# Optimization experiments

Hardware: AMD Instinct MI355X
Metric: run time of the kernel (lower is better)

The kernel has to match this reference:

```python
import jax, jax.numpy as jnp
import numpy as np

B, S, E, H, W = 1, 4096, 1024, 16, 256
D = E // H
SCALE = D ** -0.5


def setup_inputs() -> dict:
    key = jax.random.key(0)
    k1, k2, k3 = jax.random.split(key, 3)
    x = jax.random.normal(k1, (B, S, E), dtype=jnp.float32)
    # torch Linear weight is [out,in]; we store transposed [in,out] so y = x @ w
    w_qkv = jax.random.normal(k2, (E, 3 * E), dtype=jnp.float32) * (E ** -0.5)
    w_out = jax.random.normal(k3, (E, E), dtype=jnp.float32) * (E ** -0.5)
    # sliding-window causal mask: key j allowed for query i iff i-W < j <= i
    q_idx = jnp.arange(S)[:, None]
    k_idx = jnp.arange(S)[None, :]
    allowed_mask = (k_idx <= q_idx) & (k_idx > q_idx - W)  # [S,S] bool
    allowed_mask = allowed_mask[None, None]  # [1,1,S,S]
    return {"x": x, "allowed_mask": allowed_mask, "w_qkv": w_qkv, "w_out": w_out}


def reference(x, allowed_mask, w_qkv, w_out):
    b, s, e = x.shape
    qkv = (x @ w_qkv).reshape(b, s, 3, H, D)
    q, k, v = jnp.moveaxis(qkv, 2, 0)  # each [b,s,H,D]
    q = q.transpose(0, 2, 1, 3)  # [b,H,s,D]
    k = k.transpose(0, 2, 1, 3)
    v = v.transpose(0, 2, 1, 3)
    scores = jnp.einsum('bhsd,bhtd->bhst', q, k) * SCALE  # [b,H,s,s]
    scores = jnp.where(allowed_mask, scores, -jnp.inf)
    attn = jax.nn.softmax(scores, axis=-1)
    out = jnp.einsum('bhst,bhtd->bhsd', attn, v)  # [b,H,s,D]
    out = out.transpose(0, 2, 1, 3).reshape(b, s, e)
    return out @ w_out
```

## Files before the change

kernel.cpp:

```cpp
#include <hip/hip_runtime.h>
#include <hip/hip_bf16.h>

#define S_LEN 4096
#define EMB   1024
#define NH    16
#define HD    64
#define WIN   256
#define SCALE 0.125f

typedef __attribute__((ext_vector_type(8))) short short8;
typedef __attribute__((ext_vector_type(4))) float f32x4;
typedef __attribute__((ext_vector_type(4))) unsigned short us4;

__device__ inline unsigned short f2b(float x) {
    __hip_bfloat16 b = __float2bfloat16(x);
    return *reinterpret_cast<unsigned short*>(&b);
}

__device__ inline void gld_lds16(const unsigned short* g, unsigned short* l) {
    __builtin_amdgcn_global_load_lds(
        (const __attribute__((address_space(1))) unsigned int*)g,
        (__attribute__((address_space(3))) unsigned int*)l,
        16, 0, 0);
}

__device__ inline void transpose_tile(const float* __restrict__ in,
                                      unsigned short* __restrict__ out,
                                      int R, int C, int bx, int by,
                                      unsigned short* t) {
    const int tid = threadIdx.x;
    const int r0 = by * 64, c0 = bx * 64;

    const int rr = tid >> 4, cc = (tid & 15) * 4;
    #pragma unroll
    for (int i = 0; i < 4; ++i) {
        float4 v = *reinterpret_cast<const float4*>(&in[(size_t)(r0 + rr + i * 16) * C + c0 + cc]);
        t[(cc + 0) * 72 + rr + i * 16] = f2b(v.x);
        t[(cc + 1) * 72 + rr + i * 16] = f2b(v.y);
        t[(cc + 2) * 72 + rr + i * 16] = f2b(v.z);
        t[(cc + 3) * 72 + rr + i * 16] = f2b(v.w);
    }
    __syncthreads();

    const int wr = tid >> 2, wk = (tid & 3) * 16;
    #pragma unroll
    for (int p = 0; p < 2; ++p)
        *reinterpret_cast<uint4*>(&out[(size_t)(c0 + wr) * R + r0 + wk + p * 8]) =
            *reinterpret_cast<const uint4*>(&t[wr * 72 + wk + p * 8]);
}

__global__ __launch_bounds__(256) void prep(const float* __restrict__ x,
                                            unsigned short* __restrict__ xb,
                                            const float* __restrict__ w_qkv,
                                            unsigned short* __restrict__ wqkvT,
                                            const float* __restrict__ w_out,
                                            unsigned short* __restrict__ woutT) {
    __shared__ alignas(16) unsigned short t[64 * 72];
    const int b = blockIdx.x;
    if (b < 768) {
        transpose_tile(w_qkv, wqkvT, EMB, 3 * EMB, b % 48, b / 48, t);
    } else if (b < 1024) {
        const int bb = b - 768;
        transpose_tile(w_out, woutT, EMB, EMB, bb & 15, bb >> 4, t);
    } else {
        const size_t tt = (size_t)(b - 1024) * 256 + threadIdx.x;
        const float4* s4 = reinterpret_cast<const float4*>(x) + tt * 4;
        float4 v0 = s4[0], v1 = s4[1], v2 = s4[2], v3 = s4[3];
        us4 p0 = {f2b(v0.x), f2b(v0.y), f2b(v0.z), f2b(v0.w)};
        us4 p1 = {f2b(v1.x), f2b(v1.y), f2b(v1.z), f2b(v1.w)};
        us4 p2 = {f2b(v2.x), f2b(v2.y), f2b(v2.z), f2b(v2.w)};
        us4 p3 = {f2b(v3.x), f2b(v3.y), f2b(v3.z), f2b(v3.w)};
        us4* d = reinterpret_cast<us4*>(xb) + tt * 4;
        d[0] = p0; d[1] = p1; d[2] = p2; d[3] = p3;
    }
}

template <int MODE, int BN>
__global__ __launch_bounds__(256) void gemm_bt(const unsigned short* __restrict__ A,
                                               const unsigned short* __restrict__ Bt,
                                               void* __restrict__ Cout,
                                               unsigned short* __restrict__ vT,
                                               int M, int N, int K) {
    constexpr int SMEM_ELEMS = (MODE == 1) ? 17408 : 8192 + BN * 64;
    constexpr int NJ = BN / 32;
    __shared__ alignas(16) unsigned short smem[SMEM_ELEMS];
    unsigned short* As = smem;
    unsigned short* Bs = smem + 8192;

    const int tid  = threadIdx.x;
    const int lane = tid & 63;
    const int w    = tid >> 6;
    const int quad = lane >> 4;
    const int l16  = lane & 15;

    const int m0 = blockIdx.y * 128;
    const int n0 = blockIdx.x * BN;
    const int m_off = (w & 1) * 64;
    const int n_off = (w >> 1) * (BN / 2);

    const int s_row = tid >> 3;
    const int s_c0  = tid & 7;

    f32x4 acc[4][NJ];
    #pragma unroll
    for (int i = 0; i < 4; ++i)
        #pragma unroll
        for (int j = 0; j < NJ; ++j)
            acc[i][j] = (f32x4){0.f, 0.f, 0.f, 0.f};

    for (int bk = 0; bk < K; bk += 64) {
        __syncthreads();
        #pragma unroll
        for (int p = 0; p < 4; ++p) {
            const int row = p * 32 + s_row;
            const int c   = s_c0 ^ (row & 7);
            gld_lds16(A + (size_t)(m0 + row) * K + bk + c * 8,
                      As + (p * 256 + w * 64) * 8);
        }
        #pragma unroll
        for (int p = 0; p < BN / 32; ++p) {
            const int row = p * 32 + s_row;
            const int c   = s_c0 ^ (row & 7);
            gld_lds16(Bt + (size_t)(n0 + row) * K + bk + c * 8,
                      Bs + (p * 256 + w * 64) * 8);
        }
        __syncthreads();

        #pragma unroll
        for (int ks = 0; ks < 2; ++ks) {
            short8 af[4], bf[NJ];
            #pragma unroll
            for (int i = 0; i < 4; ++i) {
                const int r = m_off + i * 16 + l16;
                af[i] = *reinterpret_cast<const short8*>(
                    &As[r * 64 + ((ks * 4 + quad) ^ (r & 7)) * 8]);
            }
            #pragma unroll
            for (int j = 0; j < NJ; ++j) {
                const int r = n_off + j * 16 + l16;
                bf[j] = *reinterpret_cast<const short8*>(
                    &Bs[r * 64 + ((ks * 4 + quad) ^ (r & 7)) * 8]);
            }
            #pragma unroll
            for (int i = 0; i < 4; ++i)
                #pragma unroll
                for (int j = 0; j < NJ; ++j)
                    acc[i][j] = __builtin_amdgcn_mfma_f32_16x16x32_bf16(
                        af[i], bf[j], acc[i][j], 0, 0, 0);
        }
    }

    if (MODE == 0) {
        float* C = (float*)Cout;
        #pragma unroll
        for (int i = 0; i < 4; ++i)
            #pragma unroll
            for (int r = 0; r < 4; ++r) {
                const size_t row = m0 + m_off + i * 16 + quad * 4 + r;
                #pragma unroll
                for (int j = 0; j < NJ; ++j)
                    C[row * N + n0 + n_off + j * 16 + l16] = acc[i][j][r];
            }
    } else if (n0 < 2048) {
        const float sc = (n0 < 1024) ? SCALE : 1.0f;
        unsigned short* C = (unsigned short*)Cout;
        #pragma unroll
        for (int i = 0; i < 4; ++i)
            #pragma unroll
            for (int r = 0; r < 4; ++r) {
                const size_t row = m0 + m_off + i * 16 + quad * 4 + r;
                #pragma unroll
                for (int j = 0; j < NJ; ++j)
                    C[row * N + n0 + n_off + j * 16 + l16] = f2b(acc[i][j][r] * sc);
            }
    } else {
        __syncthreads();
        #pragma unroll
        for (int i = 0; i < 4; ++i) {
            const int ss = m_off + i * 16 + quad * 4;
            #pragma unroll
            for (int j = 0; j < NJ; ++j) {
                const int dd = n_off + j * 16 + l16;
                us4 pk = {f2b(acc[i][j][0]), f2b(acc[i][j][1]),
                          f2b(acc[i][j][2]), f2b(acc[i][j][3])};
                *reinterpret_cast<us4*>(&smem[dd * 136 + ss]) = pk;
            }
        }
        __syncthreads();
        #pragma unroll
        for (int p = 0; p < 8; ++p) {
            const int t  = p * 256 + tid;
            const int dd = t >> 4;
            const int sc2 = (t & 15) * 8;
            *reinterpret_cast<uint4*>(&vT[(size_t)(n0 - 2048 + dd) * S_LEN + m0 + sc2]) =
                *reinterpret_cast<const uint4*>(&smem[dd * 136 + sc2]);
        }
    }
}

__global__ __launch_bounds__(512) void gemm_qkv(const unsigned short* __restrict__ A,
                                                const unsigned short* __restrict__ Bt,
                                                unsigned short* __restrict__ C,
                                                unsigned short* __restrict__ vT) {
    __shared__ alignas(16) unsigned short smem[65536];

    constexpr int K = EMB;
    const int tid  = threadIdx.x;
    const int lane = tid & 63;
    const int w    = tid >> 6;
    const int quad = lane >> 4;
    const int l16  = lane & 15;
    const int wr   = w >> 2, wc = w & 3;
    const int wm0  = wr * 128, wn0 = wc * 64;

    const int raw = blockIdx.x;
    const int s   = (raw & 7) * 24 + (raw >> 3);
    const int by  = s / 12, bx = s % 12;
    const int m0  = by * 256, n0 = bx * 256;

    const int srow = tid >> 2;
    const int scp  = tid & 3;
    const int sc4  = scp ^ ((srow >> 1) & 3);
    const unsigned short* pA = A  + (size_t)(m0 + srow) * K + sc4 * 8;
    const unsigned short* pB = Bt + (size_t)(n0 + srow) * K + sc4 * 8;
    const int dls = (w * 64) * 8;

    auto STAGE = [&](int q) {
        unsigned short* dA = smem + ((q >> 1) & 1) * 32768 + (q & 1) * 8192 + dls;
        unsigned short* dB = dA + 16384;
        const int gk = q * 32;
        gld_lds16(pA + gk, dA);
        gld_lds16(pA + (size_t)128 * K + gk, dA + 4096);
        gld_lds16(pB + gk, dB);
        gld_lds16(pB + (size_t)128 * K + gk, dB + 4096);
    };

    auto BASE = [&](int p) -> const unsigned short* {
        return smem + ((p >> 1) & 1) * 32768 + (p & 1) * 8192;
    };

    const int cpf = quad ^ ((l16 >> 1) & 3);
    const int oA  = (wm0 + l16) * 32 + cpf * 8;
    const int oB  = (wn0 + l16) * 32 + cpf * 8;

    f32x4 acc[8][4];
    #pragma unroll
    for (int i = 0; i < 8; ++i)
        #pragma unroll
        for (int j = 0; j < 4; ++j)
            acc[i][j] = (f32x4){0.f, 0.f, 0.f, 0.f};

    short8 afA[8], afB[8];

#define PHASE_RR(p, CUR, NXT, DO_PF, DO_ST) do {                               \
    const unsigned short* Bb_ = BASE(p) + 16384;                               \
    short8 bf[4];                                                              \
    _Pragma("unroll")                                                          \
    for (int j = 0; j < 4; ++j)                                                \
        bf[j] = *reinterpret_cast<const short8*>(&Bb_[oB + j * 512]);          \
    if (DO_PF) {                                                               \
        const unsigned short* An_ = BASE((p) + 1);                             \
        _Pragma("unroll")                                                      \
        for (int i = 0; i < 8; ++i)                                            \
            NXT[i] = *reinterpret_cast<const short8*>(&An_[oA + i * 512]);     \
    }                                                                          \
    if (DO_ST) STAGE((p) + 3);                                                 \
    __builtin_amdgcn_s_setprio(1);                                             \
    _Pragma("unroll")                                                          \
    for (int j = 0; j < 4; ++j)                                                \
        _Pragma("unroll")                                                      \
        for (int i = 0; i < 8; ++i)                                            \
            acc[i][j] = __builtin_amdgcn_mfma_f32_16x16x32_bf16(               \
                CUR[i], bf[j], acc[i][j], 0, 0, 0);                            \
    __builtin_amdgcn_s_setprio(0);                                             \
} while (0)

    STAGE(0); STAGE(1); STAGE(2);
    asm volatile("s_waitcnt vmcnt(4)" ::: "memory");
    __builtin_amdgcn_s_barrier();
    {
        const unsigned short* A0_ = BASE(0);
        #pragma unroll
        for (int i = 0; i < 8; ++i)
            afA[i] = *reinterpret_cast<const short8*>(&A0_[oA + i * 512]);
    }

    for (int pp = 0; pp < 28; pp += 2) {
        PHASE_RR(pp, afA, afB, true, true);
        asm volatile("s_waitcnt vmcnt(4)" ::: "memory");
        __builtin_amdgcn_s_barrier();
        PHASE_RR(pp + 1, afB, afA, true, true);
        asm volatile("s_waitcnt vmcnt(4)" ::: "memory");
        __builtin_amdgcn_s_barrier();
    }
    PHASE_RR(28, afA, afB, true, true);
    asm volatile("s_waitcnt vmcnt(4)" ::: "memory");
    __builtin_amdgcn_s_barrier();
    PHASE_RR(29, afB, afA, true, false);
    asm volatile("s_waitcnt vmcnt(0)" ::: "memory");
    __builtin_amdgcn_s_barrier();
    PHASE_RR(30, afA, afB, true, false);
    __builtin_amdgcn_s_barrier();
    PHASE_RR(31, afB, afA, false, false);
    __builtin_amdgcn_s_barrier();

#undef PHASE_RR

    const int sec = n0 >> 10;
    if (sec < 2) {
        const float sc = (sec == 0) ? SCALE : 1.0f;
        #pragma unroll
        for (int i = 0; i < 8; ++i) {
            #pragma unroll
            for (int r = 0; r < 4; ++r) {
                const size_t row = (size_t)(m0 + wm0 + i * 16 + quad * 4 + r) * 3072;
                #pragma unroll
                for (int j = 0; j < 4; ++j)
                    C[row + n0 + wn0 + j * 16 + l16] = f2b(acc[i][j][r] * sc);
            }
        }
    } else {
        #pragma unroll
        for (int i = 0; i < 8; ++i) {
            const int ss = wm0 + i * 16 + quad * 4;
            const int sc0 = ss >> 3, se = ss & 7;
            #pragma unroll
            for (int j = 0; j < 4; ++j) {
                const int d = wn0 + j * 16 + l16;
                us4 pk = {f2b(acc[i][j][0]), f2b(acc[i][j][1]),
                          f2b(acc[i][j][2]), f2b(acc[i][j][3])};
                *reinterpret_cast<us4*>(&smem[d * 256 + ((sc0 ^ (d & 31)) << 3) + se]) = pk;
            }
        }
        __builtin_amdgcn_s_barrier();
        const int vb = n0 - 2048;
        #pragma unroll
        for (int rep = 0; rep < 16; ++rep) {
            const int idx = rep * 512 + tid;
            const int d = idx >> 5, scr = idx & 31;
            *reinterpret_cast<uint4*>(&vT[(size_t)(vb + d) * S_LEN + m0 + scr * 8]) =
                *reinterpret_cast<const uint4*>(&smem[d * 256 + ((scr ^ (d & 31)) << 3)]);
        }
    }
}

typedef __attribute__((ext_vector_type(2))) unsigned int u32x2;

template <int PAR>
__device__ __forceinline__ void pv_phase(const u32x2 (&PA)[17], unsigned short* scrw,
                                         const unsigned short* Vt, f32x4 (&acco)[4],
                                         int ks0, int quad, int l16, short8 af) {
    const int wq  = quad & 1;
    const int tlq = quad >> 1;
    #pragma unroll
    for (int ksi = 0; ksi < 9; ++ksi) {
        if (ksi == 2) { asm volatile("s_waitcnt vmcnt(5)" ::: "memory"); __builtin_amdgcn_s_barrier(); }
        if (ksi == 4) { asm volatile("s_waitcnt vmcnt(3)" ::: "memory"); __builtin_amdgcn_s_barrier(); }
        if (ksi == 6) { asm volatile("s_waitcnt vmcnt(1)" ::: "memory"); __builtin_amdgcn_s_barrier(); }
        if (ksi == 8) { asm volatile("s_waitcnt vmcnt(0)" ::: "memory"); __builtin_amdgcn_s_barrier(); }
        const int ks = ks0 + ksi;
        if (ksi < 8) {
            #pragma unroll
            for (int tl = 0; tl < 2; ++tl) {
                const int nb = 2 * (ksi + 1) + tl - PAR;
                u32x2 v = (nb >= 0 && nb <= 16) ? PA[(nb < 0) ? 0 : ((nb > 16) ? 16 : nb)]
                                                : (u32x2){0u, 0u};
                *reinterpret_cast<u32x2*>(&scrw[((ksi + 1) & 1) * 768 + tl * 384 + l16 * 24 + quad * 4]) = v;
            }
        }
        #pragma unroll
        for (int nb2 = 0; nb2 < 4; ++nb2) {
            const int d = nb2 * 16 + l16;
            const short8 bfr = *reinterpret_cast<const short8*>(
                &Vt[ks * 2048 + d * 32 + ((quad ^ ((d >> 1) & 3)) << 3)]);
            acco[nb2] = __builtin_amdgcn_mfma_f32_16x16x32_bf16(af, bfr, acco[nb2], 0, 0, 0);
        }
        if (ksi < 8)
            af = *reinterpret_cast<const short8*>(&scrw[((ksi + 1) & 1) * 768 + tlq * 384 + l16 * 24 + wq * 8]);
    }
}

__global__ __launch_bounds__(256, 3) void attn_mfma(const unsigned short* __restrict__ qkv,
                                                    const unsigned short* __restrict__ vT,
                                                    unsigned short* __restrict__ outb) {
    __shared__ alignas(16) unsigned short lds[26624];
    unsigned short* KtV = lds;
    unsigned short* scr = lds + 20480;

    const int raw  = blockIdx.x + (blockIdx.y << 6);
    const int xcd  = raw & 7;
    const int slot = raw >> 3;
    const int q0   = (xcd * 8 + (slot & 7)) * 64;
    const int h    = slot >> 3;

    const int tid  = threadIdx.x;
    const int w    = tid >> 6;
    const int lane = tid & 63;
    const int quad = lane >> 4;
    const int l16  = lane & 15;
    const int kbase = q0 - 256;

    const unsigned short* qrow = qkv + (size_t)(q0 + w * 16 + l16) * 3072 + h * 64;
    short8 aq[2];
    aq[0] = *reinterpret_cast<const short8*>(qrow + quad * 8);
    aq[1] = *reinterpret_cast<const short8*>(qrow + 32 + quad * 8);

    #pragma unroll
    for (int i = 0; i < 10; ++i) {
        const int fc  = i * 256 + tid;
        const int row = fc >> 3, p = fc & 7;
        const int c   = p ^ (row & 7);
        int j = kbase + row; if (j < 0) j = 0;
        gld_lds16(qkv + (size_t)j * 3072 + EMB + h * 64 + c * 8,
                  KtV + (i * 256 + w * 64) * 8);
    }

    __syncthreads();

    const int iq = q0 + w * 16 + l16;
    float rsum = 0.f;
    u32x2 PA[17];
    #pragma unroll
    for (int nb = 0; nb < 17; ++nb) {
        const int row = (w + nb) * 16 + l16;
        f32x4 acc = (f32x4){0.f, 0.f, 0.f, 0.f};
        #pragma unroll
        for (int ks = 0; ks < 2; ++ks) {
            const int p = (ks * 4 + quad) ^ (l16 & 7);
            const short8 kf = *reinterpret_cast<const short8*>(&KtV[row * 64 + p * 8]);
            acc = __builtin_amdgcn_mfma_f32_16x16x32_bf16(kf, aq[ks], acc, 0, 0, 0);
        }
        const int jb = kbase + (w + nb) * 16 + quad * 4;
        float ev0, ev1, ev2, ev3;
        {
            const int j0 = jb, j1 = jb + 1, j2 = jb + 2, j3 = jb + 3;
            ev0 = ((j0 >= 0) & (j0 <= iq) & (j0 > iq - WIN)) ? __expf(acc[0]) : 0.f;
            ev1 = ((j1 >= 0) & (j1 <= iq) & (j1 > iq - WIN)) ? __expf(acc[1]) : 0.f;
            ev2 = ((j2 >= 0) & (j2 <= iq) & (j2 > iq - WIN)) ? __expf(acc[2]) : 0.f;
            ev3 = ((j3 >= 0) & (j3 <= iq) & (j3 > iq - WIN)) ? __expf(acc[3]) : 0.f;
        }
        rsum += (ev0 + ev1) + (ev2 + ev3);
        PA[nb][0] = ((unsigned)f2b(ev1) << 16) | f2b(ev0);
        PA[nb][1] = ((unsigned)f2b(ev3) << 16) | f2b(ev2);
    }
    rsum += __shfl_xor(rsum, 16, 64);
    rsum += __shfl_xor(rsum, 32, 64);
    const float inv_l = 1.f / rsum;

    __syncthreads();

    {
        const int vd  = tid >> 2;
        const int vpo = tid & 3;
        const int vsw = vpo ^ ((vd >> 1) & 3);
        const unsigned short* vsrc = vT + (size_t)(h * 64 + vd) * S_LEN;
        #pragma unroll
        for (int i = 0; i < 10; ++i) {
            int j0 = kbase + (4 * i + vsw) * 8; if (j0 < 0) j0 = 0;
            gld_lds16(vsrc + j0, KtV + (i * 256 + w * 64) * 8);
        }
    }

    unsigned short* scrw = scr + w * 1536;
    const int par = w & 1;
    {
        const u32x2 z = {0u, 0u};
        u32x2 v0 = par ? z : PA[0];
        u32x2 v1 = par ? PA[0] : PA[1];
        *reinterpret_cast<u32x2*>(&scrw[0 * 384 + l16 * 24 + quad * 4]) = v0;
        *reinterpret_cast<u32x2*>(&scrw[1 * 384 + l16 * 24 + quad * 4]) = v1;
    }
    const short8 af0 = *reinterpret_cast<const short8*>(
        &scrw[(quad >> 1) * 384 + l16 * 24 + (quad & 1) * 8]);

    asm volatile("s_waitcnt vmcnt(7)" ::: "memory");
    __builtin_amdgcn_s_barrier();

    f32x4 acco[4];
    #pragma unroll
    for (int nb2 = 0; nb2 < 4; ++nb2) acco[nb2] = (f32x4){0.f, 0.f, 0.f, 0.f};

    const int ks0 = w >> 1;
    if (par == 0) pv_phase<0>(PA, scrw, KtV, acco, ks0, quad, l16, af0);
    else          pv_phase<1>(PA, scrw, KtV, acco, ks0, quad, l16, af0);

    float invo[4];
    #pragma unroll
    for (int r = 0; r < 4; ++r)
        invo[r] = __shfl(inv_l, quad * 4 + r, 64);

    #pragma unroll
    for (int nb2 = 0; nb2 < 4; ++nb2)
        #pragma unroll
        for (int r = 0; r < 4; ++r)
            outb[(size_t)(q0 + w * 16 + quad * 4 + r) * EMB + h * 64 + nb2 * 16 + l16] =
                f2b(acco[nb2][r] * invo[r]);
}

extern "C" void kernel_launch(void* const* d_in, const int* in_sizes, int n_in,
                              void* d_out, int out_size, void* d_ws, size_t ws_size,
                              hipStream_t stream) {
    const float* x     = (const float*)d_in[0];
    const float* w_qkv = (const float*)d_in[2];
    const float* w_out = (const float*)d_in[3];
    float* out = (float*)d_out;

    char* ws = (char*)d_ws;
    unsigned short* xb     = (unsigned short*)(ws);
    unsigned short* wqkvT  = (unsigned short*)(ws + (8u  << 20));
    unsigned short* woutT  = (unsigned short*)(ws + (14u << 20));
    unsigned short* qkvb   = (unsigned short*)(ws + (16u << 20));
    unsigned short* attnb  = (unsigned short*)(ws + (48u << 20));
    unsigned short* vT     = (unsigned short*)(ws + (56u << 20));

    prep<<<2048, 256, 0, stream>>>(x, xb, w_qkv, wqkvT, w_out, woutT);

    gemm_qkv<<<dim3(192), 512, 0, stream>>>(xb, wqkvT, qkvb, vT);

    attn_mfma<<<dim3(S_LEN / 64, NH), 256, 0, stream>>>(qkvb, vT, attnb);

    gemm_bt<0, 64><<<dim3(EMB / 64, S_LEN / 128), 256, 0, stream>>>(
        attnb, woutT, out, nullptr, S_LEN, EMB, EMB);
}
```

Baseline: 181.2 us.

## Run QKV GEMM with 1024 threads per block and smaller per-wave tiles

Doubles the QKV GEMM block from 512 to 1024 threads (16 waves), halving each wave's M tile from 128 to 64 rows so the accumulators shrink from 8x4 to 4x4. The LDS staging becomes a simple 4-slot ring where each thread loads one A and one B chunk per stage. The register double-buffered A-fragment prefetch is dropped in favour of loading A and B fragments at the start of each phase. The aim is more waves to hide latency and lower register pressure, at the cost of more LDS reads per MFMA and less prefetch overlap.

```diff
diff --git a/kernel.cpp b/kernel.cpp
--- a/kernel.cpp
+++ b/kernel.cpp
@@ -198,10 +198,10 @@
     }
 }
 
-__global__ __launch_bounds__(512) void gemm_qkv(const unsigned short* __restrict__ A,
-                                                const unsigned short* __restrict__ Bt,
-                                                unsigned short* __restrict__ C,
-                                                unsigned short* __restrict__ vT) {
+__global__ __launch_bounds__(1024, 4) void gemm_qkv(const unsigned short* __restrict__ A,
+                                                    const unsigned short* __restrict__ Bt,
+                                                    unsigned short* __restrict__ C,
+                                                    unsigned short* __restrict__ vT) {
     __shared__ alignas(16) unsigned short smem[65536];
 
     constexpr int K = EMB;
@@ -211,7 +211,7 @@
     const int quad = lane >> 4;
     const int l16  = lane & 15;
     const int wr   = w >> 2, wc = w & 3;
-    const int wm0  = wr * 128, wn0 = wc * 64;
+    const int wm0  = wr * 64, wn0 = wc * 64;
 
     const int raw = blockIdx.x;
     const int s   = (raw & 7) * 24 + (raw >> 3);
@@ -226,91 +226,62 @@
     const int dls = (w * 64) * 8;
 
     auto STAGE = [&](int q) {
-        unsigned short* dA = smem + ((q >> 1) & 1) * 32768 + (q & 1) * 8192 + dls;
-        unsigned short* dB = dA + 16384;
+        unsigned short* dA = smem + (q & 3) * 16384 + dls;
         const int gk = q * 32;
         gld_lds16(pA + gk, dA);
-        gld_lds16(pA + (size_t)128 * K + gk, dA + 4096);
-        gld_lds16(pB + gk, dB);
-        gld_lds16(pB + (size_t)128 * K + gk, dB + 4096);
-    };
-
-    auto BASE = [&](int p) -> const unsigned short* {
-        return smem + ((p >> 1) & 1) * 32768 + (p & 1) * 8192;
+        gld_lds16(pB + gk, dA + 8192);
     };
 
     const int cpf = quad ^ ((l16 >> 1) & 3);
     const int oA  = (wm0 + l16) * 32 + cpf * 8;
     const int oB  = (wn0 + l16) * 32 + cpf * 8;
 
-    f32x4 acc[8][4];
-    #pragma unroll
-    for (int i = 0; i < 8; ++i)
+    f32x4 acc[4][4];
+    #pragma unroll
+    for (int i = 0; i < 4; ++i)
         #pragma unroll
         for (int j = 0; j < 4; ++j)
             acc[i][j] = (f32x4){0.f, 0.f, 0.f, 0.f};
 
-    short8 afA[8], afB[8];
-
-#define PHASE_RR(p, CUR, NXT, DO_PF, DO_ST) do {                               \
-    const unsigned short* Bb_ = BASE(p) + 16384;                               \
-    short8 bf[4];                                                              \
+#define QKV_PH(p, DO_ST, VM) do {                                              \
+    const unsigned short* Ab_ = smem + ((p) & 3) * 16384;                      \
+    const unsigned short* Bb_ = Ab_ + 8192;                                    \
+    short8 af[4], bf[4];                                                       \
+    _Pragma("unroll")                                                          \
+    for (int i = 0; i < 4; ++i)                                                \
+        af[i] = *reinterpret_cast<const short8*>(&Ab_[oA + i * 512]);          \
     _Pragma("unroll")                                                          \
     for (int j = 0; j < 4; ++j)                                                \
         bf[j] = *reinterpret_cast<const short8*>(&Bb_[oB + j * 512]);          \
-    if (DO_PF) {                                                               \
-        const unsigned short* An_ = BASE((p) + 1);                             \
-        _Pragma("unroll")                                                      \
-        for (int i = 0; i < 8; ++i)                                            \
-            NXT[i] = *reinterpret_cast<const short8*>(&An_[oA + i * 512]);     \
-    }                                                                          \
     if (DO_ST) STAGE((p) + 3);                                                 \
     __builtin_amdgcn_s_setprio(1);                                             \
     _Pragma("unroll")                                                          \
-    for (int j = 0; j < 4; ++j)                                                \
+    for (int i = 0; i < 4; ++i)                                                \
         _Pragma("unroll")                                                      \
-        for (int i = 0; i < 8; ++i)                                            \
+        for (int j = 0; j < 4; ++j)                                            \
             acc[i][j] = __builtin_amdgcn_mfma_f32_16x16x32_bf16(               \
-                CUR[i], bf[j], acc[i][j], 0, 0, 0);                            \
+                af[i], bf[j], acc[i][j], 0, 0, 0);                             \
     __builtin_amdgcn_s_setprio(0);                                             \
+    asm volatile("s_waitcnt " VM ::: "memory");                                \
+    __builtin_amdgcn_s_barrier();                                              \
 } while (0)
 
     STAGE(0); STAGE(1); STAGE(2);
     asm volatile("s_waitcnt vmcnt(4)" ::: "memory");
     __builtin_amdgcn_s_barrier();
-    {
-        const unsigned short* A0_ = BASE(0);
-        #pragma unroll
-        for (int i = 0; i < 8; ++i)
-            afA[i] = *reinterpret_cast<const short8*>(&A0_[oA + i * 512]);
-    }
-
-    for (int pp = 0; pp < 28; pp += 2) {
-        PHASE_RR(pp, afA, afB, true, true);
-        asm volatile("s_waitcnt vmcnt(4)" ::: "memory");
-        __builtin_amdgcn_s_barrier();
-        PHASE_RR(pp + 1, afB, afA, true, true);
-        asm volatile("s_waitcnt vmcnt(4)" ::: "memory");
-        __builtin_amdgcn_s_barrier();
-    }
-    PHASE_RR(28, afA, afB, true, true);
-    asm volatile("s_waitcnt vmcnt(4)" ::: "memory");
-    __builtin_amdgcn_s_barrier();
-    PHASE_RR(29, afB, afA, true, false);
-    asm volatile("s_waitcnt vmcnt(0)" ::: "memory");
-    __builtin_amdgcn_s_barrier();
-    PHASE_RR(30, afA, afB, true, false);
-    __builtin_amdgcn_s_barrier();
-    PHASE_RR(31, afB, afA, false, false);
-    __builtin_amdgcn_s_barrier();
-
-#undef PHASE_RR
+
+    for (int p = 0; p < 29; ++p)
+        QKV_PH(p, true, "vmcnt(4)");
+    QKV_PH(29, false, "vmcnt(2)");
+    QKV_PH(30, false, "vmcnt(0)");
+    QKV_PH(31, false, "vmcnt(0)");
+#undef QKV_PH
 
     const int sec = n0 >> 10;
     if (sec < 2) {
         const float sc = (sec == 0) ? SCALE : 1.0f;
         #pragma unroll
-        for (int i = 0; i < 8; ++i) {
+        for (int i = 0; i < 4; ++i) {
             #pragma unroll
             for (int r = 0; r < 4; ++r) {
                 const size_t row = (size_t)(m0 + wm0 + i * 16 + quad * 4 + r) * 3072;
@@ -321,7 +292,7 @@
         }
     } else {
         #pragma unroll
-        for (int i = 0; i < 8; ++i) {
+        for (int i = 0; i < 4; ++i) {
             const int ss = wm0 + i * 16 + quad * 4;
             const int sc0 = ss >> 3, se = ss & 7;
             #pragma unroll
@@ -335,8 +306,8 @@
         __builtin_amdgcn_s_barrier();
         const int vb = n0 - 2048;
         #pragma unroll
-        for (int rep = 0; rep < 16; ++rep) {
-            const int idx = rep * 512 + tid;
+        for (int rep = 0; rep < 8; ++rep) {
+            const int idx = rep * 1024 + tid;
             const int d = idx >> 5, scr = idx & 31;
             *reinterpret_cast<uint4*>(&vT[(size_t)(vb + d) * S_LEN + m0 + scr * 8]) =
                 *reinterpret_cast<const uint4*>(&smem[d * 256 + ((scr ^ (d & 31)) << 3)]);
@@ -515,7 +486,7 @@
 
     prep<<<2048, 256, 0, stream>>>(x, xb, w_qkv, wqkvT, w_out, woutT);
 
-    gemm_qkv<<<dim3(192), 512, 0, stream>>>(xb, wqkvT, qkvb, vT);
+    gemm_qkv<<<dim3(192), 1024, 0, stream>>>(xb, wqkvT, qkvb, vT);
 
     attn_mfma<<<dim3(S_LEN / 64, NH), 256, 0, stream>>>(qkvb, vT, attnb);
 
```

Result: no change. 180.6 us (median of 2 runs) (-0.4%).
